# Kernel tuning notes

Hardware: AMD Instinct MI355X
Metric: run time of the kernel (lower is better)

## Reference

```python
import jax, jax.numpy as jnp
import numpy as np

N_NODES = 100000
N_EDGES = 1600000
IN_CH = 128
OUT_CH = 128
N_REL = 8


def setup_inputs() -> dict:
    key = jax.random.key(0)
    k1, k2, k3, k4, k5, k6 = jax.random.split(key, 6)
    x = jax.random.normal(k1, (N_NODES, IN_CH), dtype=jnp.float32)
    edge_index = jax.random.randint(k2, (2, N_EDGES), 0, N_NODES, dtype=jnp.int64)
    edge_type = jax.random.randint(k3, (N_EDGES,), 0, N_REL, dtype=jnp.int64)
    # learned parameters (PyG RGCNConv: per-relation weight, root weight, bias)
    scale = 1.0 / np.sqrt(IN_CH)
    weight = jax.random.normal(k4, (N_REL, IN_CH, OUT_CH), dtype=jnp.float32) * scale
    root = jax.random.normal(k5, (IN_CH, OUT_CH), dtype=jnp.float32) * scale
    bias = jax.random.normal(k6, (OUT_CH,), dtype=jnp.float32) * 0.01
    return {"x": x, "edge_index": edge_index, "edge_type": edge_type,
            "weight": weight, "root": root, "bias": bias}


def reference(x, edge_index, edge_type, weight, root, bias):
    # PyG RGCNConv forward: out_i = x_i @ root + bias
    #   + sum_r mean_{j in N_r(i)} (x_j @ W_r)   (default aggr='mean' per relation)
    N = x.shape[0]
    R, _, O = weight.shape
    src, dst = edge_index[0], edge_index[1]
    # transform all nodes under every relation once: [R, N, O]
    xW = jnp.einsum('ni,rio->rno', x, weight)
    msg = xW[edge_type, src]                      # [E, O] per-edge message
    seg = edge_type * N + dst                     # segment per (relation, dst)
    sums = jax.ops.segment_sum(msg, seg, num_segments=R * N)        # [R*N, O]
    cnt = jax.ops.segment_sum(jnp.ones_like(msg[:, 0]), seg, num_segments=R * N)
    mean = sums / jnp.maximum(cnt, 1.0)[:, None]
    agg = mean.reshape(R, N, O).sum(axis=0)       # sum over relations
    return agg + x @ root + bias
```

## Files before the change

kernel.cpp:

```cpp
#include <hip/hip_runtime.h>
#include <hip/hip_bf16.h>
#include <stdint.h>

#define N_NODES 100000
#define N_EDGES 1600000
#define CH 128
#define N_REL 8
#define N_PAD 100096
#define N_KEYS (N_NODES * N_REL)

#define NBKT 782
#define NCHUNK 782
#define CHUNK_E 2048
#define OFFS_STRIDE 784
#define PERM_LDS_CAP 4096

using frag_ab = __attribute__((ext_vector_type(8))) short;
using frag_cd = __attribute__((ext_vector_type(4))) float;

__device__ __forceinline__ short f2bs(float f) {
    union { __hip_bfloat16 h; short s; } u;
    u.h = __float2bfloat16(f);
    return u.s;
}

__device__ __forceinline__ uint32_t pack2bf(float a, float b) {
    union { __hip_bfloat16 h; unsigned short s; } ua, ub;
    ua.h = __float2bfloat16(a); ub.h = __float2bfloat16(b);
    return (uint32_t)ua.s | ((uint32_t)ub.s << 16);
}

__device__ __forceinline__ float bf_lo(uint32_t u) { return __uint_as_float(u << 16); }
__device__ __forceinline__ float bf_hi(uint32_t u) { return __uint_as_float(u & 0xffff0000u); }


__global__ __launch_bounds__(256)
void prep_kernel(const int* __restrict__ ei, const int* __restrict__ et,
                 uint32_t* __restrict__ ents, int* __restrict__ offs,
                 const float* __restrict__ x, short* __restrict__ xb,
                 const float* __restrict__ root, const float* __restrict__ W,
                 short* __restrict__ Bsw) {
    __shared__ uint32_t esave[CHUNK_E];
    __shared__ uint32_t csave[CHUNK_E];
    __shared__ short bsave[CHUNK_E];
    __shared__ int cnt[NBKT];
    __shared__ int scan_t[256];
    const int tid = threadIdx.x;
    const int c = blockIdx.x;
    const int g = blockIdx.x * 256 + tid;

    if (g < 9 * 2048) {
        int chunk = g >> 11, entry = g & 2047;
        int m16 = entry & 15, ct = (entry >> 4) & 7, quad = (entry >> 7) & 3, ks = entry >> 9;
        const float* src = (chunk == 0) ? root : W + (size_t)(chunk - 1) * CH * CH;
        int col = ct * 16 + m16, kb = ks * 32 + quad * 8;
        frag_ab f;
#pragma unroll
        for (int j = 0; j < 8; ++j) f[j] = f2bs(src[(size_t)(kb + j) * CH + col]);
        *(frag_ab*)(Bsw + (size_t)g * 8) = f;
    }

    {
        const int nst = NCHUNK * 256;
        const float4* xp = (const float4*)x;
        for (int gi = g; gi < N_NODES * CH / 8; gi += nst) {
            float4 a = xp[(size_t)gi * 2], bb = xp[(size_t)gi * 2 + 1];
            frag_ab f;
            f[0] = f2bs(a.x); f[1] = f2bs(a.y); f[2] = f2bs(a.z); f[3] = f2bs(a.w);
            f[4] = f2bs(bb.x); f[5] = f2bs(bb.y); f[6] = f2bs(bb.z); f[7] = f2bs(bb.w);
            *(frag_ab*)(xb + (size_t)gi * 8) = f;
        }
    }

    for (int i = tid; i < NBKT; i += 256) cnt[i] = 0;
    __syncthreads();
#pragma unroll
    for (int j = 0; j < 8; ++j) {
        const int li = j * 256 + tid;
        const int e = c * CHUNK_E + li;
        if (e < N_EDGES) {
            const int dst = ei[N_EDGES + e];
            const int src = ei[e];
            const int r = et[e];
            const int b = dst >> 7;
            atomicAdd(&cnt[b], 1);
            esave[li] = ((uint32_t)src << 10) | ((uint32_t)(dst & 127) << 3) | (uint32_t)r;
            bsave[li] = (short)b;
        } else {
            bsave[li] = -1;
        }
    }
    __syncthreads();
    const int b4 = 4 * tid;
    int c0 = (b4 < NBKT) ? cnt[b4] : 0;
    int c1 = (b4 + 1 < NBKT) ? cnt[b4 + 1] : 0;
    int c2 = (b4 + 2 < NBKT) ? cnt[b4 + 2] : 0;
    int c3 = (b4 + 3 < NBKT) ? cnt[b4 + 3] : 0;
    const int s4 = c0 + c1 + c2 + c3;
    scan_t[tid] = s4;
    __syncthreads();
    for (int st = 1; st < 256; st <<= 1) {
        int u = (tid >= st) ? scan_t[tid - st] : 0;
        __syncthreads();
        scan_t[tid] += u;
        __syncthreads();
    }
    const int excl = scan_t[tid] - s4;
    const int total = scan_t[255];
    {
        const int o0 = excl, o1 = o0 + c0, o2 = o1 + c1, o3 = o2 + c2;
        int* og = offs + (size_t)c * OFFS_STRIDE;
        if (b4 < NBKT)     { cnt[b4]     = o0; og[b4]     = o0; }
        if (b4 + 1 < NBKT) { cnt[b4 + 1] = o1; og[b4 + 1] = o1; }
        if (b4 + 2 < NBKT) { cnt[b4 + 2] = o2; og[b4 + 2] = o2; }
        if (b4 + 3 < NBKT) { cnt[b4 + 3] = o3; og[b4 + 3] = o3; }
        if (tid == 0) og[NBKT] = total;
    }
    __syncthreads();
#pragma unroll
    for (int j = 0; j < 8; ++j) {
        const int li = j * 256 + tid;
        const int b = bsave[li];
        if (b >= 0) {
            const int pos = atomicAdd(&cnt[b], 1);
            csave[pos] = esave[li];
        }
    }
    __syncthreads();
    {
        const uint4* cs = (const uint4*)csave;
        uint4* dg = (uint4*)(ents + (size_t)c * CHUNK_E);
#pragma unroll
        for (int i = 0; i < 2; ++i) dg[tid + 256 * i] = cs[tid + 256 * i];
    }
}

#define ACC_U4(U, B)                                            \
    do {                                                        \
        a[(B)+0] += bf_lo((U).x); a[(B)+1] += bf_hi((U).x);     \
        a[(B)+2] += bf_lo((U).y); a[(B)+3] += bf_hi((U).y);     \
        a[(B)+4] += bf_lo((U).z); a[(B)+5] += bf_hi((U).z);     \
        a[(B)+6] += bf_lo((U).w); a[(B)+7] += bf_hi((U).w);     \
    } while (0)

__global__ __launch_bounds__(512, 4)
void rgcn_fused(const uint32_t* __restrict__ ents, const int* __restrict__ offs,
                const short* __restrict__ xb, const short* __restrict__ Bsw,
                const float* __restrict__ bias, float* __restrict__ out) {
    __shared__ short Ash[128 * 128];
    __shared__ int perm_lds[PERM_LDS_CAP];
    __shared__ int lends[1025];
    __shared__ int soff[NCHUNK];
    __shared__ int slen[NCHUNK];
    __shared__ int sbase[NCHUNK];
    uint32_t* stage  = (uint32_t*)Ash;
    int*      hist   = (int*)Ash + 4096;
    int*      cursor = (int*)Ash + 5120;
    int*      shl    = (int*)Ash + 6144;

    const int tid = threadIdx.x;
    const int wave = tid >> 6, lane = tid & 63;
    const int m16 = lane & 15, quad = lane >> 4;
    const int wm = wave >> 2, wn = wave & 3;
    const int b = blockIdx.x;
    const long B0 = (long)b * 128;

    for (int c = tid; c < NCHUNK; c += 512) {
        const int s = offs[(size_t)c * OFFS_STRIDE + b];
        const int e = offs[(size_t)c * OFFS_STRIDE + b + 1];
        soff[c] = s;
        slen[c] = e - s;
    }
    hist[tid] = 0; hist[tid + 512] = 0;
    if (tid == 0) perm_lds[0] = 0;
    __syncthreads();
    int n_tot;
    {
        const int t2 = 2 * tid;
        const int l0 = (t2 < NCHUNK) ? slen[t2] : 0;
        const int l1 = (t2 + 1 < NCHUNK) ? slen[t2 + 1] : 0;
        const int ls = l0 + l1;
        shl[tid] = ls;
        __syncthreads();
        for (int st = 1; st < 512; st <<= 1) {
            int u = (tid >= st) ? shl[tid - st] : 0;
            __syncthreads();
            shl[tid] += u;
            __syncthreads();
        }
        const int lexcl = shl[tid] - ls;
        if (t2 < NCHUNK)     sbase[t2]     = lexcl;
        if (t2 + 1 < NCHUNK) sbase[t2 + 1] = lexcl + l0;
        __syncthreads();
        n_tot = shl[511];
        if (n_tot > PERM_LDS_CAP) n_tot = PERM_LDS_CAP;
    }
#pragma unroll
    for (int k = 0; k < 2; ++k) {
        const int c = 2 * tid + k;
        if (c < NCHUNK) {
            const int s = soff[c], nc = slen[c], base = sbase[c];
            const uint32_t* srcp = ents + (size_t)c * CHUNK_E + s;
            for (int i = 0; i < nc; ++i) {
                const int pos = base + i;
                if (pos < PERM_LDS_CAP) stage[pos] = srcp[i];
            }
        }
    }
    __syncthreads();
    for (int i = tid; i < n_tot; i += 512) atomicAdd(&hist[stage[i] & 1023], 1);
    __syncthreads();
    {
        const int h0 = hist[2 * tid], h1 = hist[2 * tid + 1];
        const int s2 = h0 + h1;
        shl[tid] = s2;
        __syncthreads();
        for (int st = 1; st < 512; st <<= 1) {
            int u = (tid >= st) ? shl[tid - st] : 0;
            __syncthreads();
            shl[tid] += u;
            __syncthreads();
        }
        const int excl = shl[tid] - s2;
        cursor[2 * tid]     = excl;
        cursor[2 * tid + 1] = excl + h0;
        if (tid == 0) lends[0] = 0;
        int e1 = excl + h0, e2 = excl + h0 + h1;
        lends[1 + 2 * tid] = (e1 > PERM_LDS_CAP) ? PERM_LDS_CAP : e1;
        lends[2 + 2 * tid] = (e2 > PERM_LDS_CAP) ? PERM_LDS_CAP : e2;
    }
    __syncthreads();
    for (int i = tid; i < n_tot; i += 512) {
        const uint32_t v = stage[i];
        const int pos = atomicAdd(&cursor[v & 1023], 1);
        if (pos < PERM_LDS_CAP) perm_lds[pos] = (int)(v >> 10);
    }

    float bcol[2];
#pragma unroll
    for (int ct = 0; ct < 2; ++ct) bcol[ct] = bias[wn * 32 + ct * 16 + m16];

    frag_cd acc[4][2];
#pragma unroll
    for (int mt = 0; mt < 4; ++mt)
#pragma unroll
        for (int ct = 0; ct < 2; ++ct) acc[mt][ct] = (frag_cd){0.f, 0.f, 0.f, 0.f};

#pragma unroll
    for (int ks = 0; ks < 4; ++ks) {
        frag_ab af[4];
#pragma unroll
        for (int mt = 0; mt < 4; ++mt)
            af[mt] = *(const frag_ab*)(xb + (B0 + wm * 64 + mt * 16 + m16) * CH + ks * 32 + quad * 8);
#pragma unroll
        for (int ct = 0; ct < 2; ++ct) {
            frag_ab bf = *(const frag_ab*)(Bsw + (size_t)((((ks * 4 + quad) * 8) + wn * 2 + ct) * 16 + m16) * 8);
#pragma unroll
            for (int mt = 0; mt < 4; ++mt)
                acc[mt][ct] = __builtin_amdgcn_mfma_f32_16x16x32_bf16(af[mt], bf, acc[mt][ct], 0, 0, 0);
        }
    }
    __syncthreads();

    const int lrow = tid >> 2;
    const int q4 = tid & 3;
    const uint32_t ch64 = (uint32_t)q4 << 6;
    const char* xbp = (const char*)xb;
    char* drow = (char*)Ash + lrow * 256;
    const int swz = lrow & 7;

    for (int r = 0; r < N_REL; ++r) {
        const int keyL = lrow * 8 + r;
        const int s = lends[keyL];
        const int e = lends[keyL + 1];
        float a[32];
#pragma unroll
        for (int i = 0; i < 32; ++i) a[i] = 0.f;
        int p0 = perm_lds[(s < e) ? s : 0];
        int p1 = perm_lds[(s + 1 < e) ? s + 1 : ((s < e) ? s : 0)];
        for (int k = s; k < e; k += 2) {
            const char* c0 = xbp + (((size_t)(uint32_t)p0 << 8) | ch64);
            const char* c1 = xbp + (((size_t)(uint32_t)p1 << 8) | ch64);
            const uint4 u0 = *(const uint4*)(c0);
            const uint4 u1 = *(const uint4*)(c0 + 16);
            const uint4 u2 = *(const uint4*)(c0 + 32);
            const uint4 u3 = *(const uint4*)(c0 + 48);
            const uint4 u4 = *(const uint4*)(c1);
            const uint4 u5 = *(const uint4*)(c1 + 16);
            const uint4 u6 = *(const uint4*)(c1 + 32);
            const uint4 u7 = *(const uint4*)(c1 + 48);
            const bool two = (k + 1 < e);
            const int kn = k + 2;
            p0 = perm_lds[(kn < e) ? kn : 0];
            p1 = perm_lds[(kn + 1 < e) ? kn + 1 : 0];
            ACC_U4(u0, 0); ACC_U4(u1, 8); ACC_U4(u2, 16); ACC_U4(u3, 24);
            if (two) { ACC_U4(u4, 0); ACC_U4(u5, 8); ACC_U4(u6, 16); ACC_U4(u7, 24); }
        }
        const int c = e - s;
        const float sc = (c > 1) ? (1.0f / (float)c) : 1.0f;
#pragma unroll
        for (int t = 0; t < 4; ++t) {
            uint4 w;
            w.x = pack2bf(a[t * 8 + 0] * sc, a[t * 8 + 1] * sc);
            w.y = pack2bf(a[t * 8 + 2] * sc, a[t * 8 + 3] * sc);
            w.z = pack2bf(a[t * 8 + 4] * sc, a[t * 8 + 5] * sc);
            w.w = pack2bf(a[t * 8 + 6] * sc, a[t * 8 + 7] * sc);
            *(uint4*)(drow + (((q4 * 4 + t) ^ swz) << 4)) = w;
        }
        __syncthreads();
        const short* Bc = Bsw + (size_t)(r + 1) * 2048 * 8;
#pragma unroll
        for (int ks = 0; ks < 4; ++ks) {
            frag_ab af[4];
#pragma unroll
            for (int mt = 0; mt < 4; ++mt) {
                const int lr = wm * 64 + mt * 16 + m16;
                af[mt] = *(const frag_ab*)((const char*)Ash + lr * 256 + (((ks * 4 + quad) ^ (lr & 7)) << 4));
            }
#pragma unroll
            for (int ct = 0; ct < 2; ++ct) {
                frag_ab bf = *(const frag_ab*)(Bc + (size_t)((((ks * 4 + quad) * 8) + wn * 2 + ct) * 16 + m16) * 8);
#pragma unroll
                for (int mt = 0; mt < 4; ++mt)
                    acc[mt][ct] = __builtin_amdgcn_mfma_f32_16x16x32_bf16(af[mt], bf, acc[mt][ct], 0, 0, 0);
            }
        }
        __syncthreads();
    }

#pragma unroll
    for (int mt = 0; mt < 4; ++mt) {
#pragma unroll
        for (int ct = 0; ct < 2; ++ct) {
            const long row0 = B0 + wm * 64 + mt * 16 + quad * 4;
            const int col = wn * 32 + ct * 16 + m16;
#pragma unroll
            for (int rg = 0; rg < 4; ++rg) {
                const long rr = row0 + rg;
                if (rr < N_NODES) out[rr * CH + col] = acc[mt][ct][rg] + bcol[ct];
            }
        }
    }
}


__global__ void count_rd_kernel(const int* __restrict__ ei, const int* __restrict__ et,
                                int* __restrict__ cnt) {
    int e = blockIdx.x * 256 + threadIdx.x;
    if (e < N_EDGES) {
        int dst = ei[N_EDGES + e];
        int r = et[e];
        atomicAdd(&cnt[r * N_NODES + dst], 1);
    }
}

__global__ void scatter_kernel(const int* __restrict__ ei, const int* __restrict__ et,
                               const float* __restrict__ x, float* __restrict__ sums,
                               int rel) {
    int gid = (blockIdx.x * 256 + threadIdx.x) >> 5;
    int lane = threadIdx.x & 31;
    int ngroups = gridDim.x * 8;
    for (int e = gid; e < N_EDGES; e += ngroups) {
        if (et[e] != rel) continue;
        int src = ei[e];
        int dst = ei[N_EDGES + e];
        float4 v = ((const float4*)(x + (size_t)src * CH))[lane];
        float* s = sums + (size_t)dst * CH + (size_t)lane * 4;
        atomicAdd(s + 0, v.x);
        atomicAdd(s + 1, v.y);
        atomicAdd(s + 2, v.z);
        atomicAdd(s + 3, v.w);
    }
}

__global__ __launch_bounds__(256, 2)
void gemm_kernel(const float* __restrict__ A, const float* __restrict__ B,
                 const float* __restrict__ bias, const int* __restrict__ cnt,
                 float* __restrict__ out, int accumulate) {
    const int wave = threadIdx.x >> 6;
    const int lane = threadIdx.x & 63;
    const int m16 = lane & 15;
    const int quad = lane >> 4;

    frag_ab bfrag[4][8];
#pragma unroll
    for (int ks = 0; ks < 4; ++ks) {
        const int kb = ks * 32 + quad * 8;
#pragma unroll
        for (int ct = 0; ct < 8; ++ct) {
            const int col = ct * 16 + m16;
            frag_ab f;
#pragma unroll
            for (int j = 0; j < 8; ++j)
                f[j] = f2bs(B[(size_t)(kb + j) * CH + col]);
            bfrag[ks][ct] = f;
        }
    }

    const int nstrips = (N_NODES + 63) / 64;
    for (int strip = blockIdx.x; strip < nstrips; strip += gridDim.x) {
        const int row = strip * 64 + wave * 16 + m16;
        const bool valid = row < N_NODES;
        float scale = 1.0f;
        if (cnt != nullptr && valid) {
            int c = cnt[row];
            if (c > 1) scale = 1.0f / (float)c;
        }
        const float4* arow = (const float4*)(A + (size_t)(valid ? row : 0) * CH);
        frag_cd acc[8];
#pragma unroll
        for (int ct = 0; ct < 8; ++ct) acc[ct] = (frag_cd){0.f, 0.f, 0.f, 0.f};
#pragma unroll
        for (int ks = 0; ks < 4; ++ks) {
            float4 a0 = arow[ks * 8 + quad * 2];
            float4 a1 = arow[ks * 8 + quad * 2 + 1];
            frag_ab af;
            af[0] = f2bs(a0.x * scale); af[1] = f2bs(a0.y * scale);
            af[2] = f2bs(a0.z * scale); af[3] = f2bs(a0.w * scale);
            af[4] = f2bs(a1.x * scale); af[5] = f2bs(a1.y * scale);
            af[6] = f2bs(a1.z * scale); af[7] = f2bs(a1.w * scale);
#pragma unroll
            for (int ct = 0; ct < 8; ++ct)
                acc[ct] = __builtin_amdgcn_mfma_f32_16x16x32_bf16(af, bfrag[ks][ct], acc[ct], 0, 0, 0);
        }
        const int obase = strip * 64 + wave * 16 + quad * 4;
#pragma unroll
        for (int ct = 0; ct < 8; ++ct) {
            const int col = ct * 16 + m16;
#pragma unroll
            for (int rg = 0; rg < 4; ++rg) {
                const int r = obase + rg;
                if (r < N_NODES) {
                    const size_t idx = (size_t)r * CH + col;
                    if (accumulate) out[idx] += acc[ct][rg];
                    else out[idx] = acc[ct][rg] + bias[col];
                }
            }
        }
    }
}

__global__ void edge_transform_kernel(const int* __restrict__ ei, const int* __restrict__ et,
                                      const float* __restrict__ x, const float* __restrict__ W,
                                      const int* __restrict__ cnt, float* __restrict__ out) {
    __shared__ float xs[CH];
    const int tid = threadIdx.x;
    for (int e = blockIdx.x; e < N_EDGES; e += gridDim.x) {
        const int src = ei[e];
        const int dst = ei[N_EDGES + e];
        const int r = et[e];
        __syncthreads();
        xs[tid] = x[(size_t)src * CH + tid];
        __syncthreads();
        const int c = cnt[r * N_NODES + dst];
        const float scale = (c > 1) ? (1.0f / (float)c) : 1.0f;
        const float* Wr = W + (size_t)r * CH * CH;
        float acc = 0.f;
#pragma unroll 8
        for (int k = 0; k < CH; ++k) acc += xs[k] * Wr[(size_t)k * CH + tid];
        atomicAdd(&out[(size_t)dst * CH + tid], acc * scale);
    }
}


static inline size_t al512(size_t x) { return (x + 511) & ~(size_t)511; }

extern "C" void kernel_launch(void* const* d_in, const int* in_sizes, int n_in,
                              void* d_out, int out_size, void* d_ws, size_t ws_size,
                              hipStream_t stream) {
    const float* x    = (const float*)d_in[0];
    const int*   ei   = (const int*)d_in[1];
    const int*   et   = (const int*)d_in[2];
    const float* W    = (const float*)d_in[3];
    const float* root = (const float*)d_in[4];
    const float* bias = (const float*)d_in[5];
    float* out = (float*)d_out;

    size_t o = 0;
    const size_t o_ents = o; o += al512((size_t)NCHUNK * CHUNK_E * 4);
    const size_t o_offs = o; o += al512((size_t)NCHUNK * OFFS_STRIDE * 4);
    const size_t o_bsw  = o; o += al512((size_t)9 * 2048 * 16);
    const size_t o_xb   = o; o += al512((size_t)N_PAD * CH * 2);
    const size_t need_t1 = o;

    const size_t cnt_bytes = (size_t)N_REL * N_NODES * sizeof(int);
    const size_t cnt_rsv   = al512(cnt_bytes);
    const size_t sums51    = (size_t)N_NODES * CH * sizeof(float);

    char* ws = (char*)d_ws;
    if (ws_size >= need_t1) {
        uint32_t* ents = (uint32_t*)(ws + o_ents);
        int*      offs = (int*)(ws + o_offs);
        short*    Bsw  = (short*)(ws + o_bsw);
        short*    xb   = (short*)(ws + o_xb);

        prep_kernel<<<NCHUNK, 256, 0, stream>>>(ei, et, ents, offs, x, xb, root, W, Bsw);
        rgcn_fused<<<NBKT, 512, 0, stream>>>(ents, offs, xb, Bsw, bias, out);
    } else if (ws_size >= cnt_rsv + sums51) {
        int*   cnt  = (int*)d_ws;
        float* sums = (float*)((char*)d_ws + cnt_rsv);
        hipMemsetAsync(cnt, 0, cnt_bytes, stream);
        count_rd_kernel<<<(N_EDGES + 255) / 256, 256, 0, stream>>>(ei, et, cnt);
        gemm_kernel<<<512, 256, 0, stream>>>(x, root, bias, nullptr, out, 0);
        for (int r = 0; r < N_REL; ++r) {
            hipMemsetAsync(sums, 0, sums51, stream);
            scatter_kernel<<<6400, 256, 0, stream>>>(ei, et, x, sums, r);
            gemm_kernel<<<512, 256, 0, stream>>>(sums, W + (size_t)r * CH * CH,
                                                 nullptr, cnt + (size_t)r * N_NODES, out, 1);
        }
    } else {
        int* cnt = (int*)d_ws;
        hipMemsetAsync(cnt, 0, cnt_bytes, stream);
        count_rd_kernel<<<(N_EDGES + 255) / 256, 256, 0, stream>>>(ei, et, cnt);
        gemm_kernel<<<512, 256, 0, stream>>>(x, root, bias, nullptr, out, 0);
        edge_transform_kernel<<<65536, CH, 0, stream>>>(ei, et, x, W, cnt, out);
    }
}
```

Baseline: 266.7 us.

## Halve bucketing chunk size, pack chunk offset/length, fuse histogram into staging

After: 267.6 us. No clear change (+0.3%).

```diff
diff --git a/kernel.cpp b/kernel.cpp
--- a/kernel.cpp
+++ b/kernel.cpp
@@ -10,8 +10,8 @@
 #define N_KEYS (N_NODES * N_REL)
 
 #define NBKT 782
-#define NCHUNK 782
-#define CHUNK_E 2048
+#define CHUNK_E 1024
+#define NCHUNK 1563
 #define OFFS_STRIDE 784
 #define PERM_LDS_CAP 4096
 
@@ -75,7 +75,7 @@
     for (int i = tid; i < NBKT; i += 256) cnt[i] = 0;
     __syncthreads();
 #pragma unroll
-    for (int j = 0; j < 8; ++j) {
+    for (int j = 0; j < 4; ++j) {
         const int li = j * 256 + tid;
         const int e = c * CHUNK_E + li;
         if (e < N_EDGES) {
@@ -118,7 +118,7 @@
     }
     __syncthreads();
 #pragma unroll
-    for (int j = 0; j < 8; ++j) {
+    for (int j = 0; j < 4; ++j) {
         const int li = j * 256 + tid;
         const int b = bsave[li];
         if (b >= 0) {
@@ -130,8 +130,7 @@
     {
         const uint4* cs = (const uint4*)csave;
         uint4* dg = (uint4*)(ents + (size_t)c * CHUNK_E);
-#pragma unroll
-        for (int i = 0; i < 2; ++i) dg[tid + 256 * i] = cs[tid + 256 * i];
+        dg[tid] = cs[tid];
     }
 }
 
@@ -150,8 +149,7 @@
     __shared__ short Ash[128 * 128];
     __shared__ int perm_lds[PERM_LDS_CAP];
     __shared__ int lends[1025];
-    __shared__ int soff[NCHUNK];
-    __shared__ int slen[NCHUNK];
+    __shared__ int spack[NCHUNK];
     __shared__ int sbase[NCHUNK];
     uint32_t* stage  = (uint32_t*)Ash;
     int*      hist   = (int*)Ash + 4096;
@@ -168,18 +166,19 @@
     for (int c = tid; c < NCHUNK; c += 512) {
         const int s = offs[(size_t)c * OFFS_STRIDE + b];
         const int e = offs[(size_t)c * OFFS_STRIDE + b + 1];
-        soff[c] = s;
-        slen[c] = e - s;
+        spack[c] = (s << 11) | (e - s);
     }
     hist[tid] = 0; hist[tid + 512] = 0;
     if (tid == 0) perm_lds[0] = 0;
     __syncthreads();
     int n_tot;
     {
-        const int t2 = 2 * tid;
-        const int l0 = (t2 < NCHUNK) ? slen[t2] : 0;
-        const int l1 = (t2 + 1 < NCHUNK) ? slen[t2 + 1] : 0;
-        const int ls = l0 + l1;
+        const int t4 = 4 * tid;
+        int l0 = (t4 < NCHUNK) ? (spack[t4] & 2047) : 0;
+        int l1 = (t4 + 1 < NCHUNK) ? (spack[t4 + 1] & 2047) : 0;
+        int l2 = (t4 + 2 < NCHUNK) ? (spack[t4 + 2] & 2047) : 0;
+        int l3 = (t4 + 3 < NCHUNK) ? (spack[t4 + 3] & 2047) : 0;
+        const int ls = l0 + l1 + l2 + l3;
         shl[tid] = ls;
         __syncthreads();
         for (int st = 1; st < 512; st <<= 1) {
@@ -189,26 +188,31 @@
             __syncthreads();
         }
         const int lexcl = shl[tid] - ls;
-        if (t2 < NCHUNK)     sbase[t2]     = lexcl;
-        if (t2 + 1 < NCHUNK) sbase[t2 + 1] = lexcl + l0;
+        if (t4 < NCHUNK)     sbase[t4]     = lexcl;
+        if (t4 + 1 < NCHUNK) sbase[t4 + 1] = lexcl + l0;
+        if (t4 + 2 < NCHUNK) sbase[t4 + 2] = lexcl + l0 + l1;
+        if (t4 + 3 < NCHUNK) sbase[t4 + 3] = lexcl + l0 + l1 + l2;
         __syncthreads();
         n_tot = shl[511];
         if (n_tot > PERM_LDS_CAP) n_tot = PERM_LDS_CAP;
     }
 #pragma unroll
-    for (int k = 0; k < 2; ++k) {
-        const int c = 2 * tid + k;
+    for (int k = 0; k < 4; ++k) {
+        const int c = 4 * tid + k;
         if (c < NCHUNK) {
-            const int s = soff[c], nc = slen[c], base = sbase[c];
+            const int sp = spack[c];
+            const int s = sp >> 11, nc = sp & 2047, base = sbase[c];
             const uint32_t* srcp = ents + (size_t)c * CHUNK_E + s;
             for (int i = 0; i < nc; ++i) {
                 const int pos = base + i;
-                if (pos < PERM_LDS_CAP) stage[pos] = srcp[i];
+                const uint32_t v = srcp[i];
+                if (pos < PERM_LDS_CAP) {
+                    stage[pos] = v;
+                    atomicAdd(&hist[v & 1023], 1);
+                }
             }
         }
     }
-    __syncthreads();
-    for (int i = tid; i < n_tot; i += 512) atomicAdd(&hist[stage[i] & 1023], 1);
     __syncthreads();
     {
         const int h0 = hist[2 * tid], h1 = hist[2 * tid + 1];
```
